# Performance work log

Hardware: AMD Instinct MI355X
Metric: run time of the kernel (lower is better)

Reference implementation:

```python
import jax, jax.numpy as jnp
import numpy as np

B, NODE, DEG, K = 16, 32, 64, 8
IN_F, OUT_F, SUP = 128, 3, 10
FEATS = [96, 256, 256, 256, 128, 128]
SIZES = [1, 2, 4, 8, 16, 32]


def setup_inputs() -> dict:
    key = jax.random.key(0)
    ks = jax.random.split(key, 20)
    d = {}
    for i in range(6):
        d[f"t{i}"] = jax.random.normal(ks[i], (B, SIZES[i], FEATS[i]), jnp.float32)
    for i in range(6):
        d[f"Wr{i}"] = jax.random.normal(ks[6 + i], (FEATS[i], OUT_F), jnp.float32) * 0.1
    d["W_branch"] = jax.random.normal(ks[12], (NODE, IN_F, DEG * IN_F), jnp.float32) * 0.02
    d["Wl1"] = jax.random.normal(ks[13], (IN_F, IN_F * SUP), jnp.float32) * 0.05
    d["Wl2"] = jax.random.normal(ks[14], (IN_F * SUP, OUT_F), jnp.float32) * 0.02
    d["bias"] = jax.random.uniform(ks[15], (1, DEG, OUT_F), jnp.float32, -0.5, 0.5)
    d["c1w"] = jax.random.normal(ks[16], (64, 6), jnp.float32) * 0.2
    d["c1b"] = jnp.zeros((64,), jnp.float32)
    d["c2w"] = jax.random.normal(ks[17], (3, 64), jnp.float32) * 0.1
    d["c2b"] = jnp.zeros((3,), jnp.float32)
    return d


def _leaky(x):
    return jnp.where(x >= 0, x, 0.2 * x)  # LeakyReLU(0.2)


def reference(t0, t1, t2, t3, t4, t5, Wr0, Wr1, Wr2, Wr3, Wr4, Wr5,
              W_branch, Wl1, Wl2, bias, c1w, c1b, c2w, c2b):
    trees = [t0, t1, t2, t3, t4, t5]
    Wrs = [Wr0, Wr1, Wr2, Wr3, Wr4, Wr5]

    # --- root aggregation: per-ancestor linear + contiguous tiling to `node` rows ---
    root = jnp.zeros((B, NODE, OUT_F), jnp.float32)
    for t, W in zip(trees, Wrs):
        rn = t.shape[1]
        root = root + jnp.repeat(t @ W, NODE // rn, axis=1)  # (B, NODE, 3)

    # --- branch upsample: per-node weight matrix, then 2-layer loop MLP ---
    branch = _leaky(jnp.einsum('bni,nio->bno', t5, W_branch))  # (B, NODE, DEG*IN_F)
    branch = branch.reshape(B, NODE * DEG, IN_F)
    branch = (branch @ Wl1) @ Wl2  # (B, N, 3)
    branch = jnp.repeat(root, DEG, axis=1) + branch  # (B, N, 3), N = NODE*DEG

    # --- EdgeConv: knn on 3-d points, gather, 1x1 convs, max over neighbors ---
    x = branch  # (B, N, 3) point coordinates
    xx = jnp.sum(x * x, axis=-1)  # (B, N)
    inner = jnp.einsum('bnc,bmc->bnm', x, x)  # (B, N, N)
    pd = 2.0 * inner - xx[:, :, None] - xx[:, None, :]  # -squared distance
    _, idx = jax.lax.top_k(pd, K)  # (B, N, K) nearest-neighbor indices

    feat = x[jnp.arange(B)[:, None, None], idx]  # (B, N, K, 3) gather
    center = jnp.broadcast_to(x[:, :, None, :], feat.shape)
    g = jnp.concatenate([feat - center, center], axis=-1)  # (B, N, K, 6)

    h = jnp.einsum('bnkc,oc->bnko', g, c1w) + c1b  # conv1 1x1: 6 -> 64
    h = jnp.einsum('bnko,po->bnkp', h, c2w) + c2b  # conv2 1x1: 64 -> 3
    h = jnp.max(h, axis=2)  # max over K neighbors -> (B, N, 3)

    out = _leaky(h + jnp.tile(bias, (1, NODE, 1)))  # bias (1, DEG, 3) tiled to (1, N, 3)
    return out
```

## Files before the change

### kernel.cpp

```cpp
#include <hip/hip_runtime.h>
#include <float.h>

#define B_    16
#define NODE_ 32
#define DEG_  64
#define KNN_  8
#define ROWS_ 2048

#define OFF_X     0
#define OFF_ROOT  131072
#define OFF_WL12  (OFF_ROOT + 2048)
#define OFF_EFF   (OFF_WL12 + 512)

__device__ __forceinline__ float med3f(float a, float b, float c) {
    return __builtin_amdgcn_fmed3f(a, b, c);
}
__device__ __forceinline__ float leaky(float v) { return v >= 0.f ? v : 0.2f * v; }

__global__ __launch_bounds__(256) void kA(
    const float* __restrict__ t0, const float* __restrict__ t1, const float* __restrict__ t2,
    const float* __restrict__ t3, const float* __restrict__ t4, const float* __restrict__ t5,
    const float* __restrict__ Wr0, const float* __restrict__ Wr1, const float* __restrict__ Wr2,
    const float* __restrict__ Wr3, const float* __restrict__ Wr4, const float* __restrict__ Wr5,
    const float* __restrict__ Wl1, const float* __restrict__ Wl2,
    const float* __restrict__ c1w, const float* __restrict__ c1b,
    const float* __restrict__ c2w, const float* __restrict__ c2b,
    float* __restrict__ ws)
{
    const int blk = blockIdx.x, tid = threadIdx.x;
    if (blk < 8) {
        const int lane = tid & 63;
        const int ibase = blk * 16 + (tid >> 6) * 4;
#pragma unroll
        for (int ii = 0; ii < 4; ++ii) {
            const float* wp = Wl1 + (size_t)(ibase + ii) * 1280;
            float a0 = 0.f, a1 = 0.f, a2 = 0.f;
            for (int s5 = 0; s5 < 20; ++s5) {
                int s = s5 * 64 + lane;
                float w = wp[s];
                a0 = fmaf(w, Wl2[s * 3 + 0], a0);
                a1 = fmaf(w, Wl2[s * 3 + 1], a1);
                a2 = fmaf(w, Wl2[s * 3 + 2], a2);
            }
#pragma unroll
            for (int d = 1; d < 64; d <<= 1) {
                a0 += __shfl_xor(a0, d);
                a1 += __shfl_xor(a1, d);
                a2 += __shfl_xor(a2, d);
            }
            if (lane == 0) {
                float* o = ws + OFF_WL12 + (ibase + ii) * 4;
                o[0] = a0; o[1] = a1; o[2] = a2; o[3] = 0.f;
            }
        }
    } else if (blk < 14) {
        int idx = (blk - 8) * 256 + tid;
        int c = idx % 3, n = (idx / 3) & 31, b = idx / 96;
        float acc = 0.f;
#define TREE(T, W, RN, F) { \
        const float* tp = T + (b * RN + ((n * RN) >> 5)) * F; \
        for (int k = 0; k < F; ++k) acc = fmaf(tp[k], W[k * 3 + c], acc); }
        TREE(t0, Wr0, 1, 96)
        TREE(t1, Wr1, 2, 256)
        TREE(t2, Wr2, 4, 256)
        TREE(t3, Wr3, 8, 256)
        TREE(t4, Wr4, 16, 128)
        TREE(t5, Wr5, 32, 128)
#undef TREE
        ws[OFF_ROOT + (b * 32 + n) * 4 + c] = acc;
    } else {
        if (tid < 18) {
            int p = tid / 6, c = tid % 6;
            float a = 0.f;
            for (int o = 0; o < 64; ++o) a = fmaf(c2w[p * 64 + o], c1w[o * 6 + c], a);
            ws[OFF_EFF + tid] = a;
        } else if (tid < 21) {
            int p = tid - 18;
            float a = c2b[p];
            for (int o = 0; o < 64; ++o) a = fmaf(c2w[p * 64 + o], c1b[o], a);
            ws[OFF_EFF + 24 + p] = a;
        }
    }
}

__global__ __launch_bounds__(256) void kBX(const float* __restrict__ t5,
                                           const float* __restrict__ Wb,
                                           float* __restrict__ ws)
{
    const int n = blockIdx.x >> 4, jt = blockIdx.x & 15, tid = threadIdx.x;
    __shared__ float ts[2048];
    for (int q = tid; q < 2048; q += 256) {
        int b = q >> 7, k = q & 127;
        ts[k * 16 + b] = t5[b * 4096 + n * 128 + k];
    }
    __syncthreads();
    const int w = tid >> 6, lane = tid & 63;
    const int d = jt * 4 + w;
    const int i0 = lane * 2;
    const float* wp = Wb + (size_t)n * 1048576 + d * 128 + i0;

    float acc[16][2];
#pragma unroll
    for (int b = 0; b < 16; ++b) { acc[b][0] = 0.f; acc[b][1] = 0.f; }

#pragma unroll 4
    for (int k = 0; k < 128; ++k) {
        float2 wv = *(const float2*)(wp + (size_t)k * 8192);
        const float4* tk = (const float4*)(ts + (k << 4));
        float4 t0v = tk[0], t1v = tk[1], t2v = tk[2], t3v = tk[3];
#define FM(BI, TV) acc[BI][0] = fmaf(TV, wv.x, acc[BI][0]); acc[BI][1] = fmaf(TV, wv.y, acc[BI][1]);
        FM(0, t0v.x) FM(1, t0v.y) FM(2, t0v.z) FM(3, t0v.w)
        FM(4, t1v.x) FM(5, t1v.y) FM(6, t1v.z) FM(7, t1v.w)
        FM(8, t2v.x) FM(9, t2v.y) FM(10, t2v.z) FM(11, t2v.w)
        FM(12, t3v.x) FM(13, t3v.y) FM(14, t3v.z) FM(15, t3v.w)
#undef FM
    }

    const float4 wl0 = *(const float4*)(ws + OFF_WL12 + i0 * 4);
    const float4 wl1 = *(const float4*)(ws + OFF_WL12 + (i0 + 1) * 4);
    float P[16][3];
#pragma unroll
    for (int b = 0; b < 16; ++b) {
        float y0 = leaky(acc[b][0]), y1 = leaky(acc[b][1]);
        P[b][0] = fmaf(y1, wl1.x, y0 * wl0.x);
        P[b][1] = fmaf(y1, wl1.y, y0 * wl0.y);
        P[b][2] = fmaf(y1, wl1.z, y0 * wl0.z);
    }
#pragma unroll
    for (int b = 0; b < 16; ++b) {
#pragma unroll
        for (int dd = 1; dd < 64; dd <<= 1) {
            P[b][0] += __shfl_xor(P[b][0], dd);
            P[b][1] += __shfl_xor(P[b][1], dd);
            P[b][2] += __shfl_xor(P[b][2], dd);
        }
    }
    float q0 = P[0][0], q1 = P[0][1], q2 = P[0][2];
#pragma unroll
    for (int b = 1; b < 16; ++b) {
        bool m = (lane == b);
        q0 = m ? P[b][0] : q0;
        q1 = m ? P[b][1] : q1;
        q2 = m ? P[b][2] : q2;
    }
    if (lane < 16) {
        float4 rt = ((const float4*)(ws + OFF_ROOT))[lane * 32 + n];
        float x0 = rt.x + q0, x1 = rt.y + q1, x2 = rt.z + q2;
        float xx = fmaf(x0, x0, fmaf(x1, x1, x2 * x2));
        ((float4*)(ws + OFF_X))[lane * 2048 + n * 64 + d] = make_float4(x0, x1, x2, xx);
    }
}

#define CAP_ 16
#define CSWAPD(a, b) { float _hi = fmaxf(a, b), _lo = fminf(a, b); a = _hi; b = _lo; }
#define INS8(P, s0,s1,s2,s3,s4,s5,s6,s7) \
    s7 = med3f(P, s7, s6); s6 = med3f(P, s6, s5); \
    s5 = med3f(P, s5, s4); s4 = med3f(P, s4, s3); \
    s3 = med3f(P, s3, s2); s2 = med3f(P, s2, s1); \
    s1 = med3f(P, s1, s0); s0 = fmaxf(s0, P);
#define MERGE8(W, s0,s1,s2,s3,s4,s5,s6,s7) { \
    float o0 = __shfl_xor(s0, W), o1 = __shfl_xor(s1, W), o2 = __shfl_xor(s2, W), o3 = __shfl_xor(s3, W); \
    float o4 = __shfl_xor(s4, W), o5 = __shfl_xor(s5, W), o6 = __shfl_xor(s6, W), o7 = __shfl_xor(s7, W); \
    float n0 = fmaxf(s0, o7), n1 = fmaxf(s1, o6), n2 = fmaxf(s2, o5), n3 = fmaxf(s3, o4); \
    float n4 = fmaxf(s4, o3), n5 = fmaxf(s5, o2), n6 = fmaxf(s6, o1), n7 = fmaxf(s7, o0); \
    CSWAPD(n0, n4) CSWAPD(n1, n5) CSWAPD(n2, n6) CSWAPD(n3, n7) \
    CSWAPD(n0, n2) CSWAPD(n1, n3) CSWAPD(n4, n6) CSWAPD(n5, n7) \
    CSWAPD(n0, n1) CSWAPD(n2, n3) CSWAPD(n4, n5) CSWAPD(n6, n7) \
    s0 = n0; s1 = n1; s2 = n2; s3 = n3; s4 = n4; s5 = n5; s6 = n6; s7 = n7; }
#define PD(XR, XM) fmaf(2.f, fmaf(XR.x, XM.x, fmaf(XR.y, XM.y, XR.z * XM.z)), -(XR.w + XM.w))

__global__ __launch_bounds__(256) void kC(const float* __restrict__ ws,
                                          const float* __restrict__ bias,
                                          float* __restrict__ out)
{
    const int bb = blockIdx.x >> 6, rtile = blockIdx.x & 63, tid = threadIdx.x;
    __shared__ float4 xs[2048];
    __shared__ float eff[32];
    __shared__ int cnt[32];
    __shared__ int lists[32][CAP_];
    __shared__ int sel[32][KNN_];

    const float4* xg = (const float4*)(ws + OFF_X) + bb * 2048;
    for (int q = tid; q < 2048; q += 256) xs[q] = xg[q];
    if (tid < 32) { eff[tid] = ws[OFF_EFF + tid]; cnt[tid] = 0; }
    __syncthreads();

    const int g  = tid >> 5;
    const int mp = tid & 31;
    const int r0 = rtile * 32 + g * 4;
    const float4 xa = xs[r0], xb = xs[r0 + 1], xc = xs[r0 + 2], xd = xs[r0 + 3];

    float A0=-FLT_MAX,A1=-FLT_MAX,A2=-FLT_MAX,A3=-FLT_MAX,A4=-FLT_MAX,A5=-FLT_MAX,A6=-FLT_MAX,A7=-FLT_MAX;
    float B0=-FLT_MAX,B1=-FLT_MAX,B2=-FLT_MAX,B3=-FLT_MAX,B4=-FLT_MAX,B5=-FLT_MAX,B6=-FLT_MAX,B7=-FLT_MAX;
    float C0=-FLT_MAX,C1=-FLT_MAX,C2=-FLT_MAX,C3=-FLT_MAX,C4=-FLT_MAX,C5=-FLT_MAX,C6=-FLT_MAX,C7=-FLT_MAX;
    float D0=-FLT_MAX,D1=-FLT_MAX,D2=-FLT_MAX,D3=-FLT_MAX,D4=-FLT_MAX,D5=-FLT_MAX,D6=-FLT_MAX,D7=-FLT_MAX;

#pragma unroll 4
    for (int mm = 0; mm < 64; ++mm) {
        float4 xm = xs[(mm << 5) | mp];
        float pa = PD(xa, xm); INS8(pa, A0,A1,A2,A3,A4,A5,A6,A7)
        float pb = PD(xb, xm); INS8(pb, B0,B1,B2,B3,B4,B5,B6,B7)
        float pc = PD(xc, xm); INS8(pc, C0,C1,C2,C3,C4,C5,C6,C7)
        float pdv = PD(xd, xm); INS8(pdv, D0,D1,D2,D3,D4,D5,D6,D7)
    }
#pragma unroll
    for (int w = 1; w < 32; w <<= 1) {
        MERGE8(w, A0,A1,A2,A3,A4,A5,A6,A7)
        MERGE8(w, B0,B1,B2,B3,B4,B5,B6,B7)
        MERGE8(w, C0,C1,C2,C3,C4,C5,C6,C7)
        MERGE8(w, D0,D1,D2,D3,D4,D5,D6,D7)
    }
    const float Ta = A7, Tb = B7, Tc = C7, Td = D7;

#pragma unroll 4
    for (int mm = 0; mm < 64; ++mm) {
        int m = (mm << 5) | mp;
        float4 xm = xs[m];
        float pa = PD(xa, xm);
        float pb = PD(xb, xm);
        float pc = PD(xc, xm);
        float pdv = PD(xd, xm);
        if (pa >= Ta) { int s = atomicAdd(&cnt[g*4+0], 1); if (s < CAP_) lists[g*4+0][s] = m | ((pa > Ta) ? 0x10000 : 0); }
        if (pb >= Tb) { int s = atomicAdd(&cnt[g*4+1], 1); if (s < CAP_) lists[g*4+1][s] = m | ((pb > Tb) ? 0x10000 : 0); }
        if (pc >= Tc) { int s = atomicAdd(&cnt[g*4+2], 1); if (s < CAP_) lists[g*4+2][s] = m | ((pc > Tc) ? 0x10000 : 0); }
        if (pdv >= Td){ int s = atomicAdd(&cnt[g*4+3], 1); if (s < CAP_) lists[g*4+3][s] = m | ((pdv > Td) ? 0x10000 : 0); }
    }
    __syncthreads();

    const int lr = tid >> 3;
    const int part = tid & 7;
    const int r = rtile * 32 + lr;
    if (part == 0) {
        int c = cnt[lr]; if (c > CAP_) c = CAP_;
        int ng = 0;
        for (int q = 0; q < c; ++q) {
            int v = lists[lr][q];
            if (v & 0x10000) sel[lr][ng++] = v & 0xFFFF;
        }
        int prev = -1;
        while (ng < KNN_) {
            int best = 0x7FFFFFFF;
            for (int q = 0; q < c; ++q) {
                int v = lists[lr][q];
                if (!(v & 0x10000)) {
                    int m = v & 0xFFFF;
                    if (m > prev && m < best) best = m;
                }
            }
            if (best == 0x7FFFFFFF) best = r;
            sel[lr][ng++] = best; prev = best;
        }
    }
    __syncthreads();

    const float4 xr = xs[r];
    const int ms = sel[lr][part];
    const float4 fm = xs[ms];
    const float g0 = fm.x - xr.x, g1 = fm.y - xr.y, g2 = fm.z - xr.z;
    float h0 = eff[24], h1 = eff[25], h2 = eff[26];
    h0 = fmaf(g0, eff[0], h0);  h0 = fmaf(g1, eff[1], h0);  h0 = fmaf(g2, eff[2], h0);
    h0 = fmaf(xr.x, eff[3], h0); h0 = fmaf(xr.y, eff[4], h0); h0 = fmaf(xr.z, eff[5], h0);
    h1 = fmaf(g0, eff[6], h1);  h1 = fmaf(g1, eff[7], h1);  h1 = fmaf(g2, eff[8], h1);
    h1 = fmaf(xr.x, eff[9], h1); h1 = fmaf(xr.y, eff[10], h1); h1 = fmaf(xr.z, eff[11], h1);
    h2 = fmaf(g0, eff[12], h2); h2 = fmaf(g1, eff[13], h2); h2 = fmaf(g2, eff[14], h2);
    h2 = fmaf(xr.x, eff[15], h2); h2 = fmaf(xr.y, eff[16], h2); h2 = fmaf(xr.z, eff[17], h2);
#pragma unroll
    for (int w = 1; w < 8; w <<= 1) {
        h0 = fmaxf(h0, __shfl_xor(h0, w));
        h1 = fmaxf(h1, __shfl_xor(h1, w));
        h2 = fmaxf(h2, __shfl_xor(h2, w));
    }
    if (part == 0) {
        const float* bp = bias + (r & 63) * 3;
        float* op = out + (size_t)(bb * 2048 + r) * 3;
        op[0] = leaky(h0 + bp[0]);
        op[1] = leaky(h1 + bp[1]);
        op[2] = leaky(h2 + bp[2]);
    }
}

extern "C" void kernel_launch(void* const* d_in, const int* in_sizes, int n_in,
                              void* d_out, int out_size, void* d_ws, size_t ws_size,
                              hipStream_t stream)
{
    const float* t0 = (const float*)d_in[0];
    const float* t1 = (const float*)d_in[1];
    const float* t2 = (const float*)d_in[2];
    const float* t3 = (const float*)d_in[3];
    const float* t4 = (const float*)d_in[4];
    const float* t5 = (const float*)d_in[5];
    const float* Wr0 = (const float*)d_in[6];
    const float* Wr1 = (const float*)d_in[7];
    const float* Wr2 = (const float*)d_in[8];
    const float* Wr3 = (const float*)d_in[9];
    const float* Wr4 = (const float*)d_in[10];
    const float* Wr5 = (const float*)d_in[11];
    const float* Wb  = (const float*)d_in[12];
    const float* Wl1 = (const float*)d_in[13];
    const float* Wl2 = (const float*)d_in[14];
    const float* bias = (const float*)d_in[15];
    const float* c1w = (const float*)d_in[16];
    const float* c1b = (const float*)d_in[17];
    const float* c2w = (const float*)d_in[18];
    const float* c2b = (const float*)d_in[19];
    float* ws = (float*)d_ws;
    float* out = (float*)d_out;

    hipLaunchKernelGGL(kA, dim3(15), dim3(256), 0, stream,
                       t0, t1, t2, t3, t4, t5, Wr0, Wr1, Wr2, Wr3, Wr4, Wr5,
                       Wl1, Wl2, c1w, c1b, c2w, c2b, ws);
    hipLaunchKernelGGL(kBX, dim3(512), dim3(256), 0, stream, t5, Wb, ws);
    hipLaunchKernelGGL(kC, dim3(1024), dim3(256), 0, stream, ws, bias, out);
}
```

Measured before the change: 326.1 us.

## Parallelize prep kernel across more blocks and simplify kNN distance scoring

The prep kernel kA goes from 15 to 161 blocks. Each Wl1·Wl2 row and each root (b,n) row now gets its own wavefront, which reduces over K with lane-strided loads and shuffle reductions instead of one thread looping over the full feature dimension. This removes a serial, poorly parallel prologue. Separately, the kNN score is rescaled to x·m − 0.5|m|², dropping the per-row norm term and the factor 2 from each distance. Ranking is unchanged, but rounding differs slightly, so ties could resolve differently.

```diff
diff --git a/kernel.cpp b/kernel.cpp
--- a/kernel.cpp
+++ b/kernel.cpp
@@ -28,38 +28,39 @@
     float* __restrict__ ws)
 {
     const int blk = blockIdx.x, tid = threadIdx.x;
-    if (blk < 8) {
-        const int lane = tid & 63;
-        const int ibase = blk * 16 + (tid >> 6) * 4;
-#pragma unroll
-        for (int ii = 0; ii < 4; ++ii) {
-            const float* wp = Wl1 + (size_t)(ibase + ii) * 1280;
-            float a0 = 0.f, a1 = 0.f, a2 = 0.f;
-            for (int s5 = 0; s5 < 20; ++s5) {
-                int s = s5 * 64 + lane;
-                float w = wp[s];
-                a0 = fmaf(w, Wl2[s * 3 + 0], a0);
-                a1 = fmaf(w, Wl2[s * 3 + 1], a1);
-                a2 = fmaf(w, Wl2[s * 3 + 2], a2);
-            }
-#pragma unroll
-            for (int d = 1; d < 64; d <<= 1) {
-                a0 += __shfl_xor(a0, d);
-                a1 += __shfl_xor(a1, d);
-                a2 += __shfl_xor(a2, d);
-            }
-            if (lane == 0) {
-                float* o = ws + OFF_WL12 + (ibase + ii) * 4;
-                o[0] = a0; o[1] = a1; o[2] = a2; o[3] = 0.f;
-            }
-        }
-    } else if (blk < 14) {
-        int idx = (blk - 8) * 256 + tid;
-        int c = idx % 3, n = (idx / 3) & 31, b = idx / 96;
-        float acc = 0.f;
+    const int w = tid >> 6, lane = tid & 63;
+    if (blk < 32) {
+        const int i = blk * 4 + w;
+        const float* wp = Wl1 + (size_t)i * 1280;
+        float a0 = 0.f, a1 = 0.f, a2 = 0.f;
+        for (int s5 = 0; s5 < 20; ++s5) {
+            int s = s5 * 64 + lane;
+            float wv = wp[s];
+            a0 = fmaf(wv, Wl2[s * 3 + 0], a0);
+            a1 = fmaf(wv, Wl2[s * 3 + 1], a1);
+            a2 = fmaf(wv, Wl2[s * 3 + 2], a2);
+        }
+#pragma unroll
+        for (int d = 1; d < 64; d <<= 1) {
+            a0 += __shfl_xor(a0, d);
+            a1 += __shfl_xor(a1, d);
+            a2 += __shfl_xor(a2, d);
+        }
+        if (lane == 0) {
+            float* o = ws + OFF_WL12 + i * 4;
+            o[0] = a0; o[1] = a1; o[2] = a2; o[3] = 0.f;
+        }
+    } else if (blk < 160) {
+        const int wv = (blk - 32) * 4 + w;
+        const int b = wv >> 5, n = wv & 31;
+        float a0 = 0.f, a1 = 0.f, a2 = 0.f;
 #define TREE(T, W, RN, F) { \
-        const float* tp = T + (b * RN + ((n * RN) >> 5)) * F; \
-        for (int k = 0; k < F; ++k) acc = fmaf(tp[k], W[k * 3 + c], acc); }
+        const float* tp = T + (size_t)(b * RN + ((n * RN) >> 5)) * F; \
+        for (int k = lane; k < F; k += 64) { \
+            float tv = tp[k]; \
+            a0 = fmaf(tv, W[k * 3 + 0], a0); \
+            a1 = fmaf(tv, W[k * 3 + 1], a1); \
+            a2 = fmaf(tv, W[k * 3 + 2], a2); } }
         TREE(t0, Wr0, 1, 96)
         TREE(t1, Wr1, 2, 256)
         TREE(t2, Wr2, 4, 256)
@@ -67,7 +68,16 @@
         TREE(t4, Wr4, 16, 128)
         TREE(t5, Wr5, 32, 128)
 #undef TREE
-        ws[OFF_ROOT + (b * 32 + n) * 4 + c] = acc;
+#pragma unroll
+        for (int d = 1; d < 64; d <<= 1) {
+            a0 += __shfl_xor(a0, d);
+            a1 += __shfl_xor(a1, d);
+            a2 += __shfl_xor(a2, d);
+        }
+        if (lane == 0) {
+            float* o = ws + OFF_ROOT + (b * 32 + n) * 4;
+            o[0] = a0; o[1] = a1; o[2] = a2;
+        }
     } else {
         if (tid < 18) {
             int p = tid / 6, c = tid % 6;
@@ -146,8 +156,8 @@
     if (lane < 16) {
         float4 rt = ((const float4*)(ws + OFF_ROOT))[lane * 32 + n];
         float x0 = rt.x + q0, x1 = rt.y + q1, x2 = rt.z + q2;
-        float xx = fmaf(x0, x0, fmaf(x1, x1, x2 * x2));
-        ((float4*)(ws + OFF_X))[lane * 2048 + n * 64 + d] = make_float4(x0, x1, x2, xx);
+        float xh = 0.5f * fmaf(x0, x0, fmaf(x1, x1, x2 * x2));
+        ((float4*)(ws + OFF_X))[lane * 2048 + n * 64 + d] = make_float4(x0, x1, x2, xh);
     }
 }
 
@@ -167,7 +177,7 @@
     CSWAPD(n0, n2) CSWAPD(n1, n3) CSWAPD(n4, n6) CSWAPD(n5, n7) \
     CSWAPD(n0, n1) CSWAPD(n2, n3) CSWAPD(n4, n5) CSWAPD(n6, n7) \
     s0 = n0; s1 = n1; s2 = n2; s3 = n3; s4 = n4; s5 = n5; s6 = n6; s7 = n7; }
-#define PD(XR, XM) fmaf(2.f, fmaf(XR.x, XM.x, fmaf(XR.y, XM.y, XR.z * XM.z)), -(XR.w + XM.w))
+#define PDQ(XR, XM) fmaf(XR.x, XM.x, fmaf(XR.y, XM.y, fmaf(XR.z, XM.z, -XM.w)))
 
 __global__ __launch_bounds__(256) void kC(const float* __restrict__ ws,
                                           const float* __restrict__ bias,
@@ -198,10 +208,10 @@
 #pragma unroll 4
     for (int mm = 0; mm < 64; ++mm) {
         float4 xm = xs[(mm << 5) | mp];
-        float pa = PD(xa, xm); INS8(pa, A0,A1,A2,A3,A4,A5,A6,A7)
-        float pb = PD(xb, xm); INS8(pb, B0,B1,B2,B3,B4,B5,B6,B7)
-        float pc = PD(xc, xm); INS8(pc, C0,C1,C2,C3,C4,C5,C6,C7)
-        float pdv = PD(xd, xm); INS8(pdv, D0,D1,D2,D3,D4,D5,D6,D7)
+        float pa = PDQ(xa, xm); INS8(pa, A0,A1,A2,A3,A4,A5,A6,A7)
+        float pb = PDQ(xb, xm); INS8(pb, B0,B1,B2,B3,B4,B5,B6,B7)
+        float pc = PDQ(xc, xm); INS8(pc, C0,C1,C2,C3,C4,C5,C6,C7)
+        float pdv = PDQ(xd, xm); INS8(pdv, D0,D1,D2,D3,D4,D5,D6,D7)
     }
 #pragma unroll
     for (int w = 1; w < 32; w <<= 1) {
@@ -216,10 +226,10 @@
     for (int mm = 0; mm < 64; ++mm) {
         int m = (mm << 5) | mp;
         float4 xm = xs[m];
-        float pa = PD(xa, xm);
-        float pb = PD(xb, xm);
-        float pc = PD(xc, xm);
-        float pdv = PD(xd, xm);
+        float pa = PDQ(xa, xm);
+        float pb = PDQ(xb, xm);
+        float pc = PDQ(xc, xm);
+        float pdv = PDQ(xd, xm);
         if (pa >= Ta) { int s = atomicAdd(&cnt[g*4+0], 1); if (s < CAP_) lists[g*4+0][s] = m | ((pa > Ta) ? 0x10000 : 0); }
         if (pb >= Tb) { int s = atomicAdd(&cnt[g*4+1], 1); if (s < CAP_) lists[g*4+1][s] = m | ((pb > Tb) ? 0x10000 : 0); }
         if (pc >= Tc) { int s = atomicAdd(&cnt[g*4+2], 1); if (s < CAP_) lists[g*4+2][s] = m | ((pc > Tc) ? 0x10000 : 0); }
@@ -306,7 +316,7 @@
     float* ws = (float*)d_ws;
     float* out = (float*)d_out;
 
-    hipLaunchKernelGGL(kA, dim3(15), dim3(256), 0, stream,
+    hipLaunchKernelGGL(kA, dim3(161), dim3(256), 0, stream,
                        t0, t1, t2, t3, t4, t5, Wr0, Wr1, Wr2, Wr3, Wr4, Wr5,
                        Wl1, Wl2, c1w, c1b, c2w, c2b, ws);
     hipLaunchKernelGGL(kBX, dim3(512), dim3(256), 0, stream, t5, Wb, ws);
```

Result: faster. 285.1 us, median of 2 (-12.5%).
